# Performance work log

Hardware: AMD Instinct MI355X
Metric: run time of the kernel (lower is better)

Reference implementation:

```python
import jax, jax.numpy as jnp
import numpy as np

N_NODES = 100000
N_EDGES = 1600000
D_IN, D_HID, N_CLASSES = 128, 128, 64


def setup_inputs() -> dict:
    key = jax.random.key(0)
    k1, k2, k3, k4 = jax.random.split(key, 4)
    x = jax.random.normal(k1, (N_NODES, D_IN), dtype=jnp.float32)
    edge_index = jax.random.randint(k2, (2, N_EDGES), 0, N_NODES, dtype=jnp.int64)
    W1 = jax.random.normal(k3, (D_IN, D_HID), dtype=jnp.float32) * 0.05
    b1 = jnp.zeros((D_HID,), dtype=jnp.float32)
    W2 = jax.random.normal(k4, (D_HID, N_CLASSES), dtype=jnp.float32) * 0.05
    b2 = jnp.zeros((N_CLASSES,), dtype=jnp.float32)
    return {"x": x, "edge_index": edge_index, "W1": W1, "b1": b1, "W2": W2, "b2": b2}


def _gcn_layer(x, src_all, dst_all, edge_w, W, b):
    # PyG GCNConv: x' = D^{-1/2} (A + I) D^{-1/2} (x W) + b
    n = x.shape[0]
    h = x @ W                                   # [N, out]
    msg = h[src_all] * edge_w[:, None]          # [E+N, out]
    out = jax.ops.segment_sum(msg, dst_all, num_segments=n)
    return out + b


def reference(x, edge_index, W1, b1, W2, b2):
    n = x.shape[0]
    src, dst = edge_index[0], edge_index[1]
    loop = jnp.arange(n, dtype=src.dtype)
    src_all = jnp.concatenate([src, loop])      # self-loops added (GCNConv default)
    dst_all = jnp.concatenate([dst, loop])
    deg = jax.ops.segment_sum(jnp.ones_like(dst_all, dtype=x.dtype), dst_all,
                              num_segments=n)
    dinv = jnp.where(deg > 0, jax.lax.rsqrt(deg), 0.0)
    edge_w = dinv[src_all] * dinv[dst_all]      # symmetric normalization

    h = _gcn_layer(x, src_all, dst_all, edge_w, W1, b1)
    h = jax.nn.relu(h)                          # dropout is identity in eval mode
    h = _gcn_layer(h, src_all, dst_all, edge_w, W2, b2)
    return jax.nn.log_softmax(h, axis=1)
```

## Files before the change

kernel.cpp:

```cpp
#include <hip/hip_runtime.h>
#include <math.h>

#define DIN 128
#define NCLS 64
#define BCAP 5120
#define SCALE1 64.0f
#define SCALE2 256.0f

typedef __attribute__((ext_vector_type(4))) float  f32x4;
typedef __attribute__((ext_vector_type(2))) float  f32x2;
typedef __attribute__((ext_vector_type(8))) short  bf16x8;

__device__ inline unsigned short f2bf(float f) {
    unsigned int u = __float_as_uint(f);
    u += 0x7fff + ((u >> 16) & 1);
    return (unsigned short)(u >> 16);
}


__global__ __launch_bounds__(256) void binA_k(const int* __restrict__ ei,
                                              int* __restrict__ gcnt,
                                              unsigned int* __restrict__ tmp,
                                              int E, int NB) {
    __shared__ int lcnt[512];
    __shared__ int gpos[512];
    const int t = threadIdx.x;
    for (int i = t; i < NB; i += 256) lcnt[i] = 0;
    __syncthreads();

    const int base = blockIdx.x * 4096;
    unsigned int pk[16];
    short bk[16], rk[16];
#pragma unroll
    for (int k = 0; k < 16; ++k) {
        int e = base + k * 256 + t;
        if (e < E) {
            int s = ei[e];
            int d = ei[E + e];
            int b = d >> 8;
            pk[k] = ((unsigned int)s << 8) | (unsigned int)(d & 255);
            bk[k] = (short)b;
            rk[k] = (short)atomicAdd(&lcnt[b], 1);
        } else {
            bk[k] = -1;
        }
    }
    __syncthreads();
    for (int i = t; i < NB; i += 256)
        gpos[i] = lcnt[i] ? atomicAdd(&gcnt[i], lcnt[i]) : 0;
    __syncthreads();
#pragma unroll
    for (int k = 0; k < 16; ++k) {
        if (bk[k] >= 0) {
            int b = bk[k];
            int pos = gpos[b] + rk[k];
            if (pos < BCAP) tmp[(size_t)b * BCAP + pos] = pk[k];
        }
    }
}

__global__ __launch_bounds__(512) void scanb_k(const int* __restrict__ gcnt,
                                               int* __restrict__ bbase, int NB) {
    __shared__ int tmp[512];
    int t = threadIdx.x;
    int v = (t < NB) ? gcnt[t] : 0;
    tmp[t] = v; __syncthreads();
    for (int o = 1; o < 512; o <<= 1) {
        int x = (t >= o) ? tmp[t - o] : 0;
        __syncthreads();
        tmp[t] += x;
        __syncthreads();
    }
    if (t < NB) bbase[t] = (t == 0) ? 0 : tmp[t - 1];
}

__global__ __launch_bounds__(256) void binB_k(const unsigned int* __restrict__ tmp,
                                              const int* __restrict__ gcnt,
                                              const int* __restrict__ bbase,
                                              int* __restrict__ off,
                                              float* __restrict__ dinv,
                                              int* __restrict__ srcs,
                                              int N, int E) {
    __shared__ unsigned int stg[BCAP];
    __shared__ int lcnt[256], sc[256], loff[256], lcur[256];
    const int b = blockIdx.x, t = threadIdx.x;
    int cnt = gcnt[b];
    if (cnt > BCAP) cnt = BCAP;
    const int base = bbase[b];
    lcnt[t] = 0; lcur[t] = 0;
    __syncthreads();
    for (int i = t; i < cnt; i += 256) {
        unsigned int v = tmp[(size_t)b * BCAP + i];
        stg[i] = v;
        atomicAdd(&lcnt[v & 255u], 1);
    }
    __syncthreads();
    sc[t] = lcnt[t]; __syncthreads();
    for (int o = 1; o < 256; o <<= 1) {
        int x = (t >= o) ? sc[t - o] : 0;
        __syncthreads();
        sc[t] += x;
        __syncthreads();
    }
    int excl = (t == 0) ? 0 : sc[t - 1];
    loff[t] = excl;
    int node = b * 256 + t;
    if (node <= N) off[node] = base + excl;
    if (node < N)  dinv[node] = rsqrtf(1.0f + (float)lcnt[t]);
    __syncthreads();
    for (int i = t; i < cnt; i += 256) {
        unsigned int v = stg[i];
        int l = v & 255u;
        int r = atomicAdd(&lcur[l], 1);
        srcs[base + loff[l] + r] = (int)(v >> 8);
    }
}


__global__ void wprep_k(const float* __restrict__ W1, const float* __restrict__ W2,
                        unsigned short* __restrict__ wt1, unsigned short* __restrict__ wt2) {
    int i = blockIdx.x * 256 + threadIdx.x;
    if (i < 128 * 128) { int k = i >> 7, n = i & 127; wt1[n * 128 + k] = f2bf(W1[i]); }
    if (i < 128 * 64)  { int k = i >> 6, n = i & 63;  wt2[n * 128 + k] = f2bf(W2[i]); }
}


template<int BN, bool AFP32>
__global__ __launch_bounds__(256) void mgemm_k(const void* __restrict__ Ap,
                                               const unsigned short* __restrict__ Bt,
                                               const float* __restrict__ dinv,
                                               unsigned char* __restrict__ C,
                                               float oscale, int N) {
    constexpr int LDK = DIN + 8;
    __shared__ unsigned short As[128 * LDK];
    __shared__ unsigned short Bs[BN * LDK];
    const int tid  = threadIdx.x;
    const int row0 = blockIdx.x * 128;

    for (int idx = tid; idx < BN * 16; idx += 256) {
        int n = idx >> 4, c = (idx & 15) << 3;
        *(uint4*)&Bs[n * LDK + c] = *(const uint4*)&Bt[n * DIN + c];
    }
    for (int idx = tid; idx < 128 * 16; idx += 256) {
        int r = idx >> 4, c = (idx & 15) << 3;
        int gr = row0 + r;
        if (AFP32) {
            unsigned short v[8];
            if (gr < N) {
                const float* A = (const float*)Ap;
                f32x4 a0 = *(const f32x4*)&A[(size_t)gr * DIN + c];
                f32x4 a1 = *(const f32x4*)&A[(size_t)gr * DIN + c + 4];
                v[0] = f2bf(a0.x); v[1] = f2bf(a0.y); v[2] = f2bf(a0.z); v[3] = f2bf(a0.w);
                v[4] = f2bf(a1.x); v[5] = f2bf(a1.y); v[6] = f2bf(a1.z); v[7] = f2bf(a1.w);
            } else {
#pragma unroll
                for (int j = 0; j < 8; ++j) v[j] = 0;
            }
            *(uint4*)&As[r * LDK + c] = *(const uint4*)v;
        } else {
            uint4 v = make_uint4(0, 0, 0, 0);
            if (gr < N) v = *(const uint4*)&((const unsigned short*)Ap)[(size_t)gr * DIN + c];
            *(uint4*)&As[r * LDK + c] = v;
        }
    }
    __syncthreads();

    const int wave = tid >> 6, lane = tid & 63;
    const int lrow = lane & 15, kq = lane >> 4;
    constexpr int NT = BN / 16;
    f32x4 acc[2][NT];
#pragma unroll
    for (int m = 0; m < 2; ++m)
#pragma unroll
        for (int t = 0; t < NT; ++t) acc[m][t] = (f32x4){0.f, 0.f, 0.f, 0.f};

    const unsigned short* Abase = &As[(wave * 32 + lrow) * LDK + kq * 8];
    const unsigned short* Bbase = &Bs[lrow * LDK + kq * 8];
#pragma unroll
    for (int kk = 0; kk < 4; ++kk) {
        bf16x8 a0 = *(const bf16x8*)(Abase + kk * 32);
        bf16x8 a1 = *(const bf16x8*)(Abase + 16 * LDK + kk * 32);
        bf16x8 bfr[NT];
#pragma unroll
        for (int t = 0; t < NT; ++t)
            bfr[t] = *(const bf16x8*)(Bbase + t * 16 * LDK + kk * 32);
#pragma unroll
        for (int t = 0; t < NT; ++t) {
            acc[0][t] = __builtin_amdgcn_mfma_f32_16x16x32_bf16(a0, bfr[t], acc[0][t], 0, 0, 0);
            acc[1][t] = __builtin_amdgcn_mfma_f32_16x16x32_bf16(a1, bfr[t], acc[1][t], 0, 0, 0);
        }
    }

#pragma unroll
    for (int tm = 0; tm < 2; ++tm) {
        int rb = row0 + wave * 32 + tm * 16 + kq * 4;
#pragma unroll
        for (int r = 0; r < 4; ++r) {
            int gr = rb + r;
            if (gr < N) {
                float sc2 = dinv[gr] * oscale;
#pragma unroll
                for (int t = 0; t < NT; t += 2) {
                    int pk = __builtin_amdgcn_cvt_pk_fp8_f32(acc[tm][t][r] * sc2,
                                                             acc[tm][t + 1][r] * sc2, 0, false);
                    C[(size_t)gr * BN + t * 16 + lrow]       = (unsigned char)(pk & 0xff);
                    C[(size_t)gr * BN + (t + 1) * 16 + lrow] = (unsigned char)((pk >> 8) & 0xff);
                }
            }
        }
    }
}

__device__ inline void dec8(uint2 v, f32x2& x0, f32x2& x1, f32x2& x2, f32x2& x3) {
    x0 += __builtin_amdgcn_cvt_pk_f32_fp8((int)v.x, false);
    x1 += __builtin_amdgcn_cvt_pk_f32_fp8((int)v.x, true);
    x2 += __builtin_amdgcn_cvt_pk_f32_fp8((int)v.y, false);
    x3 += __builtin_amdgcn_cvt_pk_f32_fp8((int)v.y, true);
}


__global__ __launch_bounds__(256) void gather1_k(const unsigned char* __restrict__ hs,
                                                 const int* __restrict__ off,
                                                 const int* __restrict__ srcs,
                                                 const float* __restrict__ dinv,
                                                 const float* __restrict__ b1,
                                                 unsigned short* __restrict__ outp, int N) {
    const int lane = threadIdx.x & 63;
    const int wave = threadIdx.x >> 6;
    const int q  = lane >> 4;
    const int ql = lane & 15;
    const int node = blockIdx.x * 16 + wave * 4 + q;
    if (node >= N) return;
    const int beg = off[node], end = off[node + 1];
    const uint2* hp = (const uint2*)hs;
    f32x2 A0 = {0.f,0.f}, A1 = {0.f,0.f}, A2 = {0.f,0.f}, A3 = {0.f,0.f};
    f32x2 C0 = {0.f,0.f}, C1 = {0.f,0.f}, C2 = {0.f,0.f}, C3 = {0.f,0.f};
    int i = beg;
    for (; i + 3 < end; i += 4) {
        unsigned s0 = (unsigned)srcs[i],     s1 = (unsigned)srcs[i + 1];
        unsigned s2 = (unsigned)srcs[i + 2], s3 = (unsigned)srcs[i + 3];
        uint2 v0 = hp[s0 * 16u + ql];
        uint2 v1 = hp[s1 * 16u + ql];
        uint2 v2 = hp[s2 * 16u + ql];
        uint2 v3 = hp[s3 * 16u + ql];
        dec8(v0, A0, A1, A2, A3);
        dec8(v1, C0, C1, C2, C3);
        dec8(v2, A0, A1, A2, A3);
        dec8(v3, C0, C1, C2, C3);
    }
    for (; i < end; ++i) {
        uint2 v = hp[(unsigned)srcs[i] * 16u + ql];
        dec8(v, A0, A1, A2, A3);
    }
    {
        uint2 v = hp[(unsigned)node * 16u + ql];
        dec8(v, C0, C1, C2, C3);
    }
    A0 += C0; A1 += C1; A2 += C2; A3 += C3;

    float d = dinv[node] * (1.0f / SCALE1);
    float4 ba = ((const float4*)b1)[ql * 2];
    float4 bb = ((const float4*)b1)[ql * 2 + 1];
    float o0 = fmaxf(fmaf(d, A0.x, ba.x), 0.f);
    float o1 = fmaxf(fmaf(d, A0.y, ba.y), 0.f);
    float o2 = fmaxf(fmaf(d, A1.x, ba.z), 0.f);
    float o3 = fmaxf(fmaf(d, A1.y, ba.w), 0.f);
    float o4 = fmaxf(fmaf(d, A2.x, bb.x), 0.f);
    float o5 = fmaxf(fmaf(d, A2.y, bb.y), 0.f);
    float o6 = fmaxf(fmaf(d, A3.x, bb.z), 0.f);
    float o7 = fmaxf(fmaf(d, A3.y, bb.w), 0.f);
    uint4 o;
    o.x = (unsigned)f2bf(o0) | ((unsigned)f2bf(o1) << 16);
    o.y = (unsigned)f2bf(o2) | ((unsigned)f2bf(o3) << 16);
    o.z = (unsigned)f2bf(o4) | ((unsigned)f2bf(o5) << 16);
    o.w = (unsigned)f2bf(o6) | ((unsigned)f2bf(o7) << 16);
    ((uint4*)outp)[(unsigned)node * 16u + ql] = o;
}


__global__ __launch_bounds__(256) void gather2_k(const unsigned char* __restrict__ hs,
                                                 const int* __restrict__ off,
                                                 const int* __restrict__ srcs,
                                                 const float* __restrict__ dinv,
                                                 const float* __restrict__ b2,
                                                 float* __restrict__ out, int N) {
    const int lane = threadIdx.x & 63;
    const int wave = threadIdx.x >> 6;
    const int o8 = lane >> 3;
    const int sl = lane & 7;
    const int node = blockIdx.x * 32 + wave * 8 + o8;
    if (node >= N) return;
    const int beg = off[node], end = off[node + 1];
    const uint2* hp = (const uint2*)hs;
    f32x2 A0 = {0.f,0.f}, A1 = {0.f,0.f}, A2 = {0.f,0.f}, A3 = {0.f,0.f};
    f32x2 C0 = {0.f,0.f}, C1 = {0.f,0.f}, C2 = {0.f,0.f}, C3 = {0.f,0.f};
    int i = beg;
    for (; i + 3 < end; i += 4) {
        unsigned s0 = (unsigned)srcs[i],     s1 = (unsigned)srcs[i + 1];
        unsigned s2 = (unsigned)srcs[i + 2], s3 = (unsigned)srcs[i + 3];
        uint2 v0 = hp[s0 * 8u + sl];
        uint2 v1 = hp[s1 * 8u + sl];
        uint2 v2 = hp[s2 * 8u + sl];
        uint2 v3 = hp[s3 * 8u + sl];
        dec8(v0, A0, A1, A2, A3);
        dec8(v1, C0, C1, C2, C3);
        dec8(v2, A0, A1, A2, A3);
        dec8(v3, C0, C1, C2, C3);
    }
    for (; i < end; ++i) {
        uint2 v = hp[(unsigned)srcs[i] * 8u + sl];
        dec8(v, A0, A1, A2, A3);
    }
    {
        uint2 v = hp[(unsigned)node * 8u + sl];
        dec8(v, C0, C1, C2, C3);
    }
    A0 += C0; A1 += C1; A2 += C2; A3 += C3;

    float d = dinv[node] * (1.0f / SCALE2);
    float4 ba = ((const float4*)b2)[sl * 2];
    float4 bb = ((const float4*)b2)[sl * 2 + 1];
    float v0 = fmaf(d, A0.x, ba.x);
    float v1 = fmaf(d, A0.y, ba.y);
    float v2 = fmaf(d, A1.x, ba.z);
    float v3 = fmaf(d, A1.y, ba.w);
    float v4 = fmaf(d, A2.x, bb.x);
    float v5 = fmaf(d, A2.y, bb.y);
    float v6 = fmaf(d, A3.x, bb.z);
    float v7 = fmaf(d, A3.y, bb.w);
    float m = fmaxf(fmaxf(fmaxf(v0, v1), fmaxf(v2, v3)), fmaxf(fmaxf(v4, v5), fmaxf(v6, v7)));
#pragma unroll
    for (int mk = 1; mk <= 4; mk <<= 1) m = fmaxf(m, __shfl_xor(m, mk, 64));
    float s = __expf(v0 - m) + __expf(v1 - m) + __expf(v2 - m) + __expf(v3 - m)
            + __expf(v4 - m) + __expf(v5 - m) + __expf(v6 - m) + __expf(v7 - m);
#pragma unroll
    for (int mk = 1; mk <= 4; mk <<= 1) s += __shfl_xor(s, mk, 64);
    float ls = m + __logf(s);
    float4 oa, ob;
    oa.x = v0 - ls; oa.y = v1 - ls; oa.z = v2 - ls; oa.w = v3 - ls;
    ob.x = v4 - ls; ob.y = v5 - ls; ob.z = v6 - ls; ob.w = v7 - ls;
    ((float4*)out)[(unsigned)node * 16u + sl * 2]     = oa;
    ((float4*)out)[(unsigned)node * 16u + sl * 2 + 1] = ob;
}


extern "C" void kernel_launch(void* const* d_in, const int* in_sizes, int n_in,
                              void* d_out, int out_size, void* d_ws, size_t ws_size,
                              hipStream_t stream) {
    const float* x  = (const float*)d_in[0];
    const int*   ei = (const int*)d_in[1];
    const float* W1 = (const float*)d_in[2];
    const float* b1 = (const float*)d_in[3];
    const float* W2 = (const float*)d_in[4];
    const float* b2 = (const float*)d_in[5];
    float* out = (float*)d_out;

    const int N  = in_sizes[0] / DIN;
    const int E  = in_sizes[1] / 2;
    const int NB = (N + 255) >> 8;

    char* p = (char*)d_ws;
    auto alloc = [&](size_t bytes) { void* r = p; p += (bytes + 255) & ~(size_t)255; return r; };
    float* dinv  = (float*)alloc((size_t)N * 4);
    int*   gcnt  = (int*)  alloc((size_t)NB * 4);
    int*   bbase = (int*)  alloc((size_t)NB * 4);
    int*   off   = (int*)  alloc((size_t)(N + 1) * 4);
    int*   srcs  = (int*)  alloc((size_t)E * 4);
    unsigned int* tmp = (unsigned int*)alloc((size_t)NB * BCAP * 4);
    unsigned short* wt1 = (unsigned short*)alloc(128 * 128 * 2);
    unsigned short* wt2 = (unsigned short*)alloc(64 * 128 * 2);
    unsigned char*  hs1 = (unsigned char*)alloc((size_t)N * DIN);
    unsigned short* h1p = (unsigned short*)alloc((size_t)N * DIN * 2);
    unsigned char*  hs2 = (unsigned char*)alloc((size_t)N * NCLS);

    wprep_k<<<64, 256, 0, stream>>>(W1, W2, wt1, wt2);
    hipMemsetAsync(gcnt, 0, (size_t)NB * 4, stream);
    binA_k<<<(E + 4095) / 4096, 256, 0, stream>>>(ei, gcnt, tmp, E, NB);
    scanb_k<<<1, 512, 0, stream>>>(gcnt, bbase, NB);
    binB_k<<<NB, 256, 0, stream>>>(tmp, gcnt, bbase, off, dinv, srcs, N, E);

    mgemm_k<DIN, true><<<(N + 127) / 128, 256, 0, stream>>>(x, wt1, dinv, hs1, SCALE1, N);
    gather1_k<<<(N + 15) / 16, 256, 0, stream>>>(hs1, off, srcs, dinv, b1, h1p, N);

    mgemm_k<NCLS, false><<<(N + 127) / 128, 256, 0, stream>>>(h1p, wt2, dinv, hs2, SCALE2, N);
    gather2_k<<<(N + 31) / 32, 256, 0, stream>>>(hs2, off, srcs, dinv, b2, out, N);
}
```

Before: 241.2 us.

## Fuse layer-1 gather with layer-2 GEMM and shrink layer-1 GEMM tile

```diff
diff --git a/kernel.cpp b/kernel.cpp
--- a/kernel.cpp
+++ b/kernel.cpp
@@ -118,94 +118,79 @@
 
 
 __global__ void wprep_k(const float* __restrict__ W1, const float* __restrict__ W2,
-                        unsigned short* __restrict__ wt1, unsigned short* __restrict__ wt2) {
+                        unsigned short* __restrict__ wt1, unsigned short* __restrict__ wt2,
+                        int* __restrict__ gcnt, int NB) {
     int i = blockIdx.x * 256 + threadIdx.x;
     if (i < 128 * 128) { int k = i >> 7, n = i & 127; wt1[n * 128 + k] = f2bf(W1[i]); }
     if (i < 128 * 64)  { int k = i >> 6, n = i & 63;  wt2[n * 128 + k] = f2bf(W2[i]); }
-}
-
-
-template<int BN, bool AFP32>
-__global__ __launch_bounds__(256) void mgemm_k(const void* __restrict__ Ap,
+    if (i < NB)        gcnt[i] = 0;
+}
+
+
+__global__ __launch_bounds__(256) void mgemm_k(const float* __restrict__ A,
                                                const unsigned short* __restrict__ Bt,
                                                const float* __restrict__ dinv,
                                                unsigned char* __restrict__ C,
                                                float oscale, int N) {
     constexpr int LDK = DIN + 8;
-    __shared__ unsigned short As[128 * LDK];
+    constexpr int BN  = 128;
+    __shared__ unsigned short As[64 * LDK];
     __shared__ unsigned short Bs[BN * LDK];
     const int tid  = threadIdx.x;
-    const int row0 = blockIdx.x * 128;
+    const int row0 = blockIdx.x * 64;
 
     for (int idx = tid; idx < BN * 16; idx += 256) {
         int n = idx >> 4, c = (idx & 15) << 3;
         *(uint4*)&Bs[n * LDK + c] = *(const uint4*)&Bt[n * DIN + c];
     }
-    for (int idx = tid; idx < 128 * 16; idx += 256) {
+    for (int idx = tid; idx < 64 * 16; idx += 256) {
         int r = idx >> 4, c = (idx & 15) << 3;
         int gr = row0 + r;
-        if (AFP32) {
-            unsigned short v[8];
-            if (gr < N) {
-                const float* A = (const float*)Ap;
-                f32x4 a0 = *(const f32x4*)&A[(size_t)gr * DIN + c];
-                f32x4 a1 = *(const f32x4*)&A[(size_t)gr * DIN + c + 4];
-                v[0] = f2bf(a0.x); v[1] = f2bf(a0.y); v[2] = f2bf(a0.z); v[3] = f2bf(a0.w);
-                v[4] = f2bf(a1.x); v[5] = f2bf(a1.y); v[6] = f2bf(a1.z); v[7] = f2bf(a1.w);
-            } else {
-#pragma unroll
-                for (int j = 0; j < 8; ++j) v[j] = 0;
-            }
-            *(uint4*)&As[r * LDK + c] = *(const uint4*)v;
+        unsigned short v[8];
+        if (gr < N) {
+            f32x4 a0 = *(const f32x4*)&A[(size_t)gr * DIN + c];
+            f32x4 a1 = *(const f32x4*)&A[(size_t)gr * DIN + c + 4];
+            v[0] = f2bf(a0.x); v[1] = f2bf(a0.y); v[2] = f2bf(a0.z); v[3] = f2bf(a0.w);
+            v[4] = f2bf(a1.x); v[5] = f2bf(a1.y); v[6] = f2bf(a1.z); v[7] = f2bf(a1.w);
         } else {
-            uint4 v = make_uint4(0, 0, 0, 0);
-            if (gr < N) v = *(const uint4*)&((const unsigned short*)Ap)[(size_t)gr * DIN + c];
-            *(uint4*)&As[r * LDK + c] = v;
-        }
+#pragma unroll
+            for (int j = 0; j < 8; ++j) v[j] = 0;
+        }
+        *(uint4*)&As[r * LDK + c] = *(const uint4*)v;
     }
     __syncthreads();
 
     const int wave = tid >> 6, lane = tid & 63;
     const int lrow = lane & 15, kq = lane >> 4;
     constexpr int NT = BN / 16;
-    f32x4 acc[2][NT];
-#pragma unroll
-    for (int m = 0; m < 2; ++m)
-#pragma unroll
-        for (int t = 0; t < NT; ++t) acc[m][t] = (f32x4){0.f, 0.f, 0.f, 0.f};
-
-    const unsigned short* Abase = &As[(wave * 32 + lrow) * LDK + kq * 8];
+    f32x4 acc[NT];
+#pragma unroll
+    for (int t = 0; t < NT; ++t) acc[t] = (f32x4){0.f, 0.f, 0.f, 0.f};
+
+    const unsigned short* Abase = &As[(wave * 16 + lrow) * LDK + kq * 8];
     const unsigned short* Bbase = &Bs[lrow * LDK + kq * 8];
 #pragma unroll
     for (int kk = 0; kk < 4; ++kk) {
-        bf16x8 a0 = *(const bf16x8*)(Abase + kk * 32);
-        bf16x8 a1 = *(const bf16x8*)(Abase + 16 * LDK + kk * 32);
-        bf16x8 bfr[NT];
-#pragma unroll
-        for (int t = 0; t < NT; ++t)
-            bfr[t] = *(const bf16x8*)(Bbase + t * 16 * LDK + kk * 32);
+        bf16x8 a = *(const bf16x8*)(Abase + kk * 32);
 #pragma unroll
         for (int t = 0; t < NT; ++t) {
-            acc[0][t] = __builtin_amdgcn_mfma_f32_16x16x32_bf16(a0, bfr[t], acc[0][t], 0, 0, 0);
-            acc[1][t] = __builtin_amdgcn_mfma_f32_16x16x32_bf16(a1, bfr[t], acc[1][t], 0, 0, 0);
-        }
-    }
-
-#pragma unroll
-    for (int tm = 0; tm < 2; ++tm) {
-        int rb = row0 + wave * 32 + tm * 16 + kq * 4;
-#pragma unroll
-        for (int r = 0; r < 4; ++r) {
-            int gr = rb + r;
-            if (gr < N) {
-                float sc2 = dinv[gr] * oscale;
-#pragma unroll
-                for (int t = 0; t < NT; t += 2) {
-                    int pk = __builtin_amdgcn_cvt_pk_fp8_f32(acc[tm][t][r] * sc2,
-                                                             acc[tm][t + 1][r] * sc2, 0, false);
-                    C[(size_t)gr * BN + t * 16 + lrow]       = (unsigned char)(pk & 0xff);
-                    C[(size_t)gr * BN + (t + 1) * 16 + lrow] = (unsigned char)((pk >> 8) & 0xff);
-                }
+            bf16x8 b = *(const bf16x8*)(Bbase + t * 16 * LDK + kk * 32);
+            acc[t] = __builtin_amdgcn_mfma_f32_16x16x32_bf16(a, b, acc[t], 0, 0, 0);
+        }
+    }
+
+    const int rb = row0 + wave * 16 + kq * 4;
+#pragma unroll
+    for (int r = 0; r < 4; ++r) {
+        int gr = rb + r;
+        if (gr < N) {
+            float sc2 = dinv[gr] * oscale;
+#pragma unroll
+            for (int t = 0; t < NT; t += 2) {
+                int pk = __builtin_amdgcn_cvt_pk_fp8_f32(acc[t][r] * sc2,
+                                                         acc[t + 1][r] * sc2, 0, false);
+                C[(size_t)gr * BN + t * 16 + lrow]       = (unsigned char)(pk & 0xff);
+                C[(size_t)gr * BN + (t + 1) * 16 + lrow] = (unsigned char)((pk >> 8) & 0xff);
             }
         }
     }
@@ -219,62 +204,118 @@
 }
 
 
-__global__ __launch_bounds__(256) void gather1_k(const unsigned char* __restrict__ hs,
-                                                 const int* __restrict__ off,
-                                                 const int* __restrict__ srcs,
-                                                 const float* __restrict__ dinv,
-                                                 const float* __restrict__ b1,
-                                                 unsigned short* __restrict__ outp, int N) {
-    const int lane = threadIdx.x & 63;
-    const int wave = threadIdx.x >> 6;
-    const int q  = lane >> 4;
-    const int ql = lane & 15;
-    const int node = blockIdx.x * 16 + wave * 4 + q;
-    if (node >= N) return;
-    const int beg = off[node], end = off[node + 1];
+__global__ __launch_bounds__(512) void fuse2_k(const unsigned char* __restrict__ hs,
+                                               const int* __restrict__ off,
+                                               const int* __restrict__ srcs,
+                                               const float* __restrict__ dinv,
+                                               const float* __restrict__ b1,
+                                               const unsigned short* __restrict__ Bt,
+                                               unsigned char* __restrict__ C,
+                                               int N) {
+    constexpr int LDK = DIN + 8;
+    __shared__ unsigned short As[128 * LDK];
+    __shared__ unsigned short Bs[NCLS * LDK];
+    const int tid  = threadIdx.x;
+    const int row0 = blockIdx.x * 128;
+
+    for (int idx = tid; idx < NCLS * 16; idx += 512) {
+        int n = idx >> 4, c = (idx & 15) << 3;
+        *(uint4*)&Bs[n * LDK + c] = *(const uint4*)&Bt[n * DIN + c];
+    }
+
+    const int qid = tid >> 4;
+    const int ql  = tid & 15;
     const uint2* hp = (const uint2*)hs;
-    f32x2 A0 = {0.f,0.f}, A1 = {0.f,0.f}, A2 = {0.f,0.f}, A3 = {0.f,0.f};
-    f32x2 C0 = {0.f,0.f}, C1 = {0.f,0.f}, C2 = {0.f,0.f}, C3 = {0.f,0.f};
-    int i = beg;
-    for (; i + 3 < end; i += 4) {
-        unsigned s0 = (unsigned)srcs[i],     s1 = (unsigned)srcs[i + 1];
-        unsigned s2 = (unsigned)srcs[i + 2], s3 = (unsigned)srcs[i + 3];
-        uint2 v0 = hp[s0 * 16u + ql];
-        uint2 v1 = hp[s1 * 16u + ql];
-        uint2 v2 = hp[s2 * 16u + ql];
-        uint2 v3 = hp[s3 * 16u + ql];
-        dec8(v0, A0, A1, A2, A3);
-        dec8(v1, C0, C1, C2, C3);
-        dec8(v2, A0, A1, A2, A3);
-        dec8(v3, C0, C1, C2, C3);
-    }
-    for (; i < end; ++i) {
-        uint2 v = hp[(unsigned)srcs[i] * 16u + ql];
-        dec8(v, A0, A1, A2, A3);
-    }
-    {
-        uint2 v = hp[(unsigned)node * 16u + ql];
-        dec8(v, C0, C1, C2, C3);
-    }
-    A0 += C0; A1 += C1; A2 += C2; A3 += C3;
-
-    float d = dinv[node] * (1.0f / SCALE1);
-    float4 ba = ((const float4*)b1)[ql * 2];
-    float4 bb = ((const float4*)b1)[ql * 2 + 1];
-    float o0 = fmaxf(fmaf(d, A0.x, ba.x), 0.f);
-    float o1 = fmaxf(fmaf(d, A0.y, ba.y), 0.f);
-    float o2 = fmaxf(fmaf(d, A1.x, ba.z), 0.f);
-    float o3 = fmaxf(fmaf(d, A1.y, ba.w), 0.f);
-    float o4 = fmaxf(fmaf(d, A2.x, bb.x), 0.f);
-    float o5 = fmaxf(fmaf(d, A2.y, bb.y), 0.f);
-    float o6 = fmaxf(fmaf(d, A3.x, bb.z), 0.f);
-    float o7 = fmaxf(fmaf(d, A3.y, bb.w), 0.f);
-    uint4 o;
-    o.x = (unsigned)f2bf(o0) | ((unsigned)f2bf(o1) << 16);
-    o.y = (unsigned)f2bf(o2) | ((unsigned)f2bf(o3) << 16);
-    o.z = (unsigned)f2bf(o4) | ((unsigned)f2bf(o5) << 16);
-    o.w = (unsigned)f2bf(o6) | ((unsigned)f2bf(o7) << 16);
-    ((uint4*)outp)[(unsigned)node * 16u + ql] = o;
+    const float4 ba = ((const float4*)b1)[ql * 2];
+    const float4 bb = ((const float4*)b1)[ql * 2 + 1];
+
+#pragma unroll
+    for (int j = 0; j < 4; ++j) {
+        const int r = qid * 4 + j;
+        const int node = row0 + r;
+        if (node < N) {
+            const int beg = off[node], end = off[node + 1];
+            f32x2 A0 = {0.f,0.f}, A1 = {0.f,0.f}, A2 = {0.f,0.f}, A3 = {0.f,0.f};
+            f32x2 C0 = {0.f,0.f}, C1 = {0.f,0.f}, C2 = {0.f,0.f}, C3 = {0.f,0.f};
+            int i = beg;
+            for (; i + 3 < end; i += 4) {
+                unsigned s0 = (unsigned)srcs[i],     s1 = (unsigned)srcs[i + 1];
+                unsigned s2 = (unsigned)srcs[i + 2], s3 = (unsigned)srcs[i + 3];
+                uint2 v0 = hp[s0 * 16u + ql];
+                uint2 v1 = hp[s1 * 16u + ql];
+                uint2 v2 = hp[s2 * 16u + ql];
+                uint2 v3 = hp[s3 * 16u + ql];
+                dec8(v0, A0, A1, A2, A3);
+                dec8(v1, C0, C1, C2, C3);
+                dec8(v2, A0, A1, A2, A3);
+                dec8(v3, C0, C1, C2, C3);
+            }
+            for (; i < end; ++i) {
+                uint2 v = hp[(unsigned)srcs[i] * 16u + ql];
+                dec8(v, A0, A1, A2, A3);
+            }
+            {
+                uint2 v = hp[(unsigned)node * 16u + ql];
+                dec8(v, C0, C1, C2, C3);
+            }
+            A0 += C0; A1 += C1; A2 += C2; A3 += C3;
+
+            float d = dinv[node] * (1.0f / SCALE1);
+            float o0 = fmaxf(fmaf(d, A0.x, ba.x), 0.f);
+            float o1 = fmaxf(fmaf(d, A0.y, ba.y), 0.f);
+            float o2 = fmaxf(fmaf(d, A1.x, ba.z), 0.f);
+            float o3 = fmaxf(fmaf(d, A1.y, ba.w), 0.f);
+            float o4 = fmaxf(fmaf(d, A2.x, bb.x), 0.f);
+            float o5 = fmaxf(fmaf(d, A2.y, bb.y), 0.f);
+            float o6 = fmaxf(fmaf(d, A3.x, bb.z), 0.f);
+            float o7 = fmaxf(fmaf(d, A3.y, bb.w), 0.f);
+            uint4 o;
+            o.x = (unsigned)f2bf(o0) | ((unsigned)f2bf(o1) << 16);
+            o.y = (unsigned)f2bf(o2) | ((unsigned)f2bf(o3) << 16);
+            o.z = (unsigned)f2bf(o4) | ((unsigned)f2bf(o5) << 16);
+            o.w = (unsigned)f2bf(o6) | ((unsigned)f2bf(o7) << 16);
+            *(uint4*)&As[r * LDK + ql * 8] = o;
+        } else {
+            uint4 z = make_uint4(0, 0, 0, 0);
+            *(uint4*)&As[r * LDK + ql * 8] = z;
+        }
+    }
+    __syncthreads();
+
+    const int wave = tid >> 6, lane = tid & 63;
+    const int lrow = lane & 15, kq = lane >> 4;
+    constexpr int NT = NCLS / 16;
+    f32x4 acc[NT];
+#pragma unroll
+    for (int t = 0; t < NT; ++t) acc[t] = (f32x4){0.f, 0.f, 0.f, 0.f};
+
+    const unsigned short* Abase = &As[(wave * 16 + lrow) * LDK + kq * 8];
+    const unsigned short* Bbase = &Bs[lrow * LDK + kq * 8];
+#pragma unroll
+    for (int kk = 0; kk < 4; ++kk) {
+        bf16x8 a = *(const bf16x8*)(Abase + kk * 32);
+#pragma unroll
+        for (int t = 0; t < NT; ++t) {
+            bf16x8 b = *(const bf16x8*)(Bbase + t * 16 * LDK + kk * 32);
+            acc[t] = __builtin_amdgcn_mfma_f32_16x16x32_bf16(a, b, acc[t], 0, 0, 0);
+        }
+    }
+
+    const int rb = row0 + wave * 16 + kq * 4;
+#pragma unroll
+    for (int r = 0; r < 4; ++r) {
+        int gr = rb + r;
+        if (gr < N) {
+            float sc2 = dinv[gr] * SCALE2;
+#pragma unroll
+            for (int t = 0; t < NT; t += 2) {
+                int pk = __builtin_amdgcn_cvt_pk_fp8_f32(acc[t][r] * sc2,
+                                                         acc[t + 1][r] * sc2, 0, false);
+                C[(size_t)gr * NCLS + t * 16 + lrow]       = (unsigned char)(pk & 0xff);
+                C[(size_t)gr * NCLS + (t + 1) * 16 + lrow] = (unsigned char)((pk >> 8) & 0xff);
+            }
+        }
+    }
 }
 
 
@@ -370,18 +411,14 @@
     unsigned short* wt1 = (unsigned short*)alloc(128 * 128 * 2);
     unsigned short* wt2 = (unsigned short*)alloc(64 * 128 * 2);
     unsigned char*  hs1 = (unsigned char*)alloc((size_t)N * DIN);
-    unsigned short* h1p = (unsigned short*)alloc((size_t)N * DIN * 2);
     unsigned char*  hs2 = (unsigned char*)alloc((size_t)N * NCLS);
 
-    wprep_k<<<64, 256, 0, stream>>>(W1, W2, wt1, wt2);
-    hipMemsetAsync(gcnt, 0, (size_t)NB * 4, stream);
+    wprep_k<<<64, 256, 0, stream>>>(W1, W2, wt1, wt2, gcnt, NB);
     binA_k<<<(E + 4095) / 4096, 256, 0, stream>>>(ei, gcnt, tmp, E, NB);
     scanb_k<<<1, 512, 0, stream>>>(gcnt, bbase, NB);
     binB_k<<<NB, 256, 0, stream>>>(tmp, gcnt, bbase, off, dinv, srcs, N, E);
 
-    mgemm_k<DIN, true><<<(N + 127) / 128, 256, 0, stream>>>(x, wt1, dinv, hs1, SCALE1, N);
-    gather1_k<<<(N + 15) / 16, 256, 0, stream>>>(hs1, off, srcs, dinv, b1, h1p, N);
-
-    mgemm_k<NCLS, false><<<(N + 127) / 128, 256, 0, stream>>>(h1p, wt2, dinv, hs2, SCALE2, N);
+    mgemm_k<<<(N + 63) / 64, 256, 0, stream>>>(x, wt1, dinv, hs1, SCALE1, N);
+    fuse2_k<<<(N + 127) / 128, 512, 0, stream>>>(hs1, off, srcs, dinv, b1, wt2, hs2, N);
     gather2_k<<<(N + 31) / 32, 256, 0, stream>>>(hs2, off, srcs, dinv, b2, out, N);
 }
```

Measured after the change: 241.9 us. No clear change (+0.3%).
